# Kernel optimization log

Hardware: AMD Instinct MI355X
Metric: run time of the kernel (lower is better)

## Reference

```python
import jax, jax.numpy as jnp
import numpy as np

N = 100000   # vertices
E = 600000   # directed edges
F = 200000   # triangle faces
CIN = 128
COUT = 128
H = 32       # metric MLP hidden
D = 3        # embedding_dim (3D metric)
TRI = D * (D + 1) // 2  # 6 params of a symmetric 3x3


def setup_inputs() -> dict:
    key = jax.random.key(0)
    ks = jax.random.split(key, 8)
    features = jax.random.normal(ks[0], (N, CIN), jnp.float32)
    vertices = jax.random.normal(ks[1], (N, 3), jnp.float32)
    edges = jax.random.randint(ks[2], (2, E), 0, N)
    faces = jax.random.randint(ks[3], (3, F), 0, N)
    # metric MLP params (edge tangent vector -> symmetric metric params)
    W1 = jax.random.normal(ks[4], (D, H), jnp.float32) / np.sqrt(D)
    b1 = jnp.zeros((H,), jnp.float32)
    W2 = jax.random.normal(ks[5], (H, TRI), jnp.float32) / np.sqrt(H)
    b2 = jnp.zeros((TRI,), jnp.float32)
    # per-vertex feature transform
    Wlin = jax.random.normal(ks[6], (CIN, COUT), jnp.float32) / np.sqrt(CIN)
    blin = jnp.zeros((COUT,), jnp.float32)
    return dict(features=features, vertices=vertices, edges=edges, faces=faces,
                W1=W1, b1=b1, W2=W2, b2=b2, Wlin=Wlin, blin=blin)


def _vertex_normals(vertices, faces):
    # area-weighted vertex normals from triangle faces
    v0, v1, v2 = vertices[faces[0]], vertices[faces[1]], vertices[faces[2]]
    fn = jnp.cross(v1 - v0, v2 - v0)                       # [F,3]
    n = jnp.zeros_like(vertices)
    n = n.at[faces[0]].add(fn).at[faces[1]].add(fn).at[faces[2]].add(fn)
    return n / (jnp.linalg.norm(n, axis=-1, keepdims=True) + 1e-8)


def _sym_from_flat(theta):
    # theta [E,6] -> symmetric [E,3,3]
    iu0, iu1 = jnp.triu_indices(D)
    S = jnp.zeros((theta.shape[0], D, D), theta.dtype)
    S = S.at[:, iu0, iu1].set(theta)
    S = S.at[:, iu1, iu0].set(theta)
    return S


def reference(features, vertices, edges, faces, W1, b1, W2, b2, Wlin, blin):
    eps = 1e-5
    src, dst = edges[0], edges[1]
    normals = _vertex_normals(vertices, faces)             # [N,3] ('tangent' info)
    d = vertices[dst] - vertices[src]                      # [E,3] edge vectors
    n_src = normals[src]
    t = d - jnp.sum(d * n_src, -1, keepdims=True) * n_src  # tangent-plane projection
    # learned metric per edge: MLP -> symmetric S, PSD metric M = S S
    h = jax.nn.relu(t @ W1 + b1)                           # [E,H]
    theta = h @ W2 + b2                                    # [E,6]
    S = _sym_from_flat(theta)                              # [E,3,3]
    M = jnp.einsum('eij,ejk->eik', S, S)                   # PSD metric
    q = jnp.einsum('ei,eij,ej->e', t, M, t)                # metric quadratic form
    w = jnp.exp(-q)                                        # positive edge weights
    # per-vertex linear, then metric-weighted mean aggregation over in-edges
    x = features @ Wlin + blin                             # [N,COUT]
    num = jax.ops.segment_sum(w[:, None] * x[src], dst, num_segments=N)
    den = jax.ops.segment_sum(w, dst, num_segments=N) + eps
    out = num / den[:, None]                               # MetricConv output
    # MetricConvBlock: manual per-feature normalization + ELU
    mu = out.mean(axis=0)
    sd = out.std(axis=0, ddof=1)                           # torch std is unbiased
    out = (out - mu) / (sd + eps)
    return jax.nn.elu(out)
```

## Files before the change

### kernel.cpp

```cpp
#include <hip/hip_runtime.h>
#include <hip/hip_bf16.h>
#include <math.h>

#define N_V 100000
#define N_E 600000
#define N_F 200000

typedef __attribute__((ext_vector_type(8))) short bf16x8;
typedef __attribute__((ext_vector_type(4))) float f32x4;

#define FUSED_BLOCKS 1563
#define FACE_BLOCKS 782
#define EDGE_BLOCKS 2344
#define PACK_BLOCKS 64

__device__ __forceinline__ unsigned short f2bf(float f) {
    unsigned int u = __builtin_bit_cast(unsigned int, f);
    u += 0x7fffu + ((u >> 16) & 1u);
    return (unsigned short)(u >> 16);
}

__global__ void k_build(const int* __restrict__ edges, const int* __restrict__ faces,
                        const float* __restrict__ Wlin,
                        int* __restrict__ head_e, int* __restrict__ next_e,
                        int* __restrict__ head_f, int* __restrict__ next_f,
                        unsigned short* __restrict__ Wb) {
    int b = blockIdx.x;
    int t = threadIdx.x;
    if (b < FACE_BLOCKS) {
        int f = b * 256 + t;
        if (f < N_F) {
            #pragma unroll
            for (int j = 0; j < 3; j++) {
                int v = faces[j * N_F + f];
                int c = 3 * f + j;
                int old = atomicExch(&head_f[v], c);
                next_f[c] = old;
            }
        }
    } else if (b < FACE_BLOCKS + EDGE_BLOCKS) {
        int e = (b - FACE_BLOCKS) * 256 + t;
        if (e < N_E) {
            int d = edges[N_E + e];
            int old = atomicExch(&head_e[d], e);
            next_e[e] = old;
        }
    } else {
        int i = (b - FACE_BLOCKS - EDGE_BLOCKS) * 256 + t;
        int j = i & 7;
        int lane = (i >> 3) & 63;
        int ct = (i >> 9) & 7;
        int kk = i >> 12;
        int k = kk * 32 + (lane >> 4) * 8 + j;
        int n = ct * 16 + (lane & 15);
        Wb[i] = f2bf(Wlin[k * 128 + n]);
    }
}

__global__ void k_vnorm(const float* __restrict__ vtx, const int* __restrict__ faces,
                        const int* __restrict__ head_f, const int* __restrict__ next_f,
                        float* __restrict__ nrm) {
    int v = blockIdx.x * 256 + threadIdx.x;
    if (v >= N_V) return;
    float nx = 0.f, ny = 0.f, nz = 0.f;
    int c = head_f[v];
    while (c >= 0) {
        int f = c / 3;
        int i0 = faces[f], i1 = faces[N_F + f], i2 = faces[2 * N_F + f];
        float ax = vtx[3 * i0], ay = vtx[3 * i0 + 1], az = vtx[3 * i0 + 2];
        float bx = vtx[3 * i1] - ax, by = vtx[3 * i1 + 1] - ay, bz = vtx[3 * i1 + 2] - az;
        float cx = vtx[3 * i2] - ax, cy = vtx[3 * i2 + 1] - ay, cz = vtx[3 * i2 + 2] - az;
        nx += by * cz - bz * cy;
        ny += bz * cx - bx * cz;
        nz += bx * cy - by * cx;
        c = next_f[c];
    }
    float inv = 1.f / (sqrtf(nx * nx + ny * ny + nz * nz) + 1e-8f);
    nrm[3 * v] = nx * inv; nrm[3 * v + 1] = ny * inv; nrm[3 * v + 2] = nz * inv;
}

__global__ void k_edge(const float* __restrict__ vtx, const int* __restrict__ edges,
                       const float* __restrict__ nrm,
                       const float* __restrict__ W1, const float* __restrict__ b1,
                       const float* __restrict__ W2, const float* __restrict__ b2,
                       float* __restrict__ wbuf) {
    __shared__ float sW1[96], sb1[32], sW2[192], sb2[6];
    int t = threadIdx.x;
    if (t < 96)  sW1[t] = W1[t];
    if (t < 32)  sb1[t] = b1[t];
    if (t < 192) sW2[t] = W2[t];
    if (t < 6)   sb2[t] = b2[t];
    __syncthreads();
    int e = blockIdx.x * blockDim.x + t;
    if (e >= N_E) return;
    int s = edges[e], d = edges[N_E + e];
    float dx = vtx[3 * d] - vtx[3 * s];
    float dy = vtx[3 * d + 1] - vtx[3 * s + 1];
    float dz = vtx[3 * d + 2] - vtx[3 * s + 2];
    float nx = nrm[3 * s], ny = nrm[3 * s + 1], nz = nrm[3 * s + 2];
    float dp = dx * nx + dy * ny + dz * nz;
    float tx = dx - dp * nx, ty = dy - dp * ny, tz = dz - dp * nz;
    float th0 = sb2[0], th1 = sb2[1], th2 = sb2[2], th3 = sb2[3], th4 = sb2[4], th5 = sb2[5];
    #pragma unroll
    for (int j = 0; j < 32; j++) {
        float h = tx * sW1[j] + ty * sW1[32 + j] + tz * sW1[64 + j] + sb1[j];
        h = fmaxf(h, 0.f);
        const float* w2r = &sW2[j * 6];
        th0 += h * w2r[0]; th1 += h * w2r[1]; th2 += h * w2r[2];
        th3 += h * w2r[3]; th4 += h * w2r[4]; th5 += h * w2r[5];
    }
    float ux = th0 * tx + th1 * ty + th2 * tz;
    float uy = th1 * tx + th3 * ty + th4 * tz;
    float uz = th2 * tx + th4 * ty + th5 * tz;
    float q = ux * ux + uy * uy + uz * uz;
    wbuf[e] = expf(-q);
}

__global__ __launch_bounds__(512) void k_fused(const float* __restrict__ feat,
                                               const int* __restrict__ edges,
                                               const int* __restrict__ head_e,
                                               const int* __restrict__ next_e,
                                               const float* __restrict__ wbuf,
                                               const unsigned short* __restrict__ Wb,
                                               const float* __restrict__ blin,
                                               float* __restrict__ out,
                                               float* __restrict__ partials) {
    __shared__ __align__(16) unsigned short At[64 * 136];
    __shared__ float gs[64];
    int t = threadIdx.x;
    int hw = t >> 5;
    int hl = t & 31;

    #pragma unroll
    for (int rep = 0; rep < 4; rep++) {
        int row = rep * 16 + hw;
        int v = blockIdx.x * 64 + row;
        float4 acc = {0.f, 0.f, 0.f, 0.f};
        float den = 0.f;
        if (v < N_V) {
            int e = head_e[v];
            while (e >= 0) {
                int s = edges[e];
                float w = wbuf[e];
                float4 f = *(const float4*)(feat + (size_t)s * 128 + 4 * hl);
                acc.x += w * f.x; acc.y += w * f.y; acc.z += w * f.z; acc.w += w * f.w;
                den += w;
                e = next_e[e];
            }
        }
        float inv = 1.f / (den + 1e-5f);
        ushort4 p;
        p.x = f2bf(acc.x * inv); p.y = f2bf(acc.y * inv);
        p.z = f2bf(acc.z * inv); p.w = f2bf(acc.w * inv);
        *(ushort4*)(&At[row * 136 + 4 * hl]) = p;
        if (hl == 0) gs[row] = den * inv;
    }
    __syncthreads();

    int ct = t >> 6;
    int lane = t & 63;
    int m = lane & 15, quad = lane >> 4;
    bf16x8 bfr[4];
    #pragma unroll
    for (int kk = 0; kk < 4; kk++)
        bfr[kk] = *(const bf16x8*)(Wb + (((kk * 8 + ct) * 64 + lane) << 3));
    float bl = blin[ct * 16 + m];
    float ssr = 0.f, qqr = 0.f;
    #pragma unroll
    for (int tile = 0; tile < 4; tile++) {
        f32x4 acc = (f32x4){0.f, 0.f, 0.f, 0.f};
        #pragma unroll
        for (int kk = 0; kk < 4; kk++) {
            bf16x8 af = *(const bf16x8*)(&At[(tile * 16 + m) * 136 + kk * 32 + quad * 8]);
            acc = __builtin_amdgcn_mfma_f32_16x16x32_bf16(af, bfr[kk], acc, 0, 0, 0);
        }
        int r0 = blockIdx.x * 64 + tile * 16;
        #pragma unroll
        for (int reg = 0; reg < 4; reg++) {
            int r = r0 + quad * 4 + reg;
            float g = gs[tile * 16 + quad * 4 + reg];
            float val = acc[reg] + bl * g;
            if (r < N_V) out[(size_t)r * 128 + ct * 16 + m] = val;
            ssr += val; qqr += val * val;
        }
    }
    ssr += __shfl_xor(ssr, 16); qqr += __shfl_xor(qqr, 16);
    ssr += __shfl_xor(ssr, 32); qqr += __shfl_xor(qqr, 32);
    if (quad == 0) {
        partials[(size_t)blockIdx.x * 256 + ct * 16 + m] = ssr;
        partials[(size_t)blockIdx.x * 256 + 128 + ct * 16 + m] = qqr;
    }
}

__global__ __launch_bounds__(64) void k_rstats(const float* __restrict__ partials,
                                               float* __restrict__ stats) {
    int c = blockIdx.x;
    int lane = threadIdx.x;
    float s = 0.f, q = 0.f;
    for (int b = lane; b < FUSED_BLOCKS; b += 64) {
        s += partials[(size_t)b * 256 + c];
        q += partials[(size_t)b * 256 + 128 + c];
    }
    #pragma unroll
    for (int off = 32; off; off >>= 1) {
        s += __shfl_down(s, off);
        q += __shfl_down(q, off);
    }
    if (lane == 0) {
        float mu = s * (1.f / N_V);
        float var = (q - s * mu) * (1.f / (N_V - 1));
        float sd = sqrtf(fmaxf(var, 0.f));
        stats[c] = mu;
        stats[128 + c] = 1.f / (sd + 1e-5f);
    }
}

__global__ void k_finalize(float* __restrict__ out, const float* __restrict__ stats) {
    int i = blockIdx.x * blockDim.x + threadIdx.x;
    if (i >= N_V * 32) return;
    float4 v = ((float4*)out)[i];
    int c0 = (i * 4) & 127;
    float mu0 = stats[c0], mu1 = stats[c0 + 1], mu2 = stats[c0 + 2], mu3 = stats[c0 + 3];
    float is0 = stats[128 + c0], is1 = stats[128 + c0 + 1], is2 = stats[128 + c0 + 2], is3 = stats[128 + c0 + 3];
    v.x = (v.x - mu0) * is0; v.y = (v.y - mu1) * is1;
    v.z = (v.z - mu2) * is2; v.w = (v.w - mu3) * is3;
    v.x = v.x > 0.f ? v.x : expm1f(v.x);
    v.y = v.y > 0.f ? v.y : expm1f(v.y);
    v.z = v.z > 0.f ? v.z : expm1f(v.z);
    v.w = v.w > 0.f ? v.w : expm1f(v.w);
    ((float4*)out)[i] = v;
}

extern "C" void kernel_launch(void* const* d_in, const int* in_sizes, int n_in,
                              void* d_out, int out_size, void* d_ws, size_t ws_size,
                              hipStream_t stream) {
    const float* feat  = (const float*)d_in[0];
    const float* vtx   = (const float*)d_in[1];
    const int*   edges = (const int*)d_in[2];
    const int*   faces = (const int*)d_in[3];
    const float* W1   = (const float*)d_in[4];
    const float* b1   = (const float*)d_in[5];
    const float* W2   = (const float*)d_in[6];
    const float* b2   = (const float*)d_in[7];
    const float* Wlin = (const float*)d_in[8];
    const float* blin = (const float*)d_in[9];
    float* out = (float*)d_out;

    float* ws = (float*)d_ws;
    int*   head_e   = (int*)ws;
    int*   head_f   = (int*)(ws + 100000);
    float* nrm      = ws + 200000;
    float* partials = ws + 100000;
    int*   next_e   = (int*)(ws + 500128);
    int*   next_f   = (int*)(ws + 1100128);
    float* wbuf     = ws + 1100128;
    unsigned short* Wb = (unsigned short*)(ws + 1700128);
    float* stats    = ws;

    hipMemsetAsync(d_ws, 0xFF, 200000 * sizeof(int), stream);

    k_build<<<FACE_BLOCKS + EDGE_BLOCKS + PACK_BLOCKS, 256, 0, stream>>>(
        edges, faces, Wlin, head_e, next_e, head_f, next_f, Wb);
    k_vnorm<<<(N_V + 255) / 256, 256, 0, stream>>>(vtx, faces, head_f, next_f, nrm);
    k_edge<<<EDGE_BLOCKS, 256, 0, stream>>>(vtx, edges, nrm, W1, b1, W2, b2, wbuf);
    k_fused<<<FUSED_BLOCKS, 512, 0, stream>>>(feat, edges, head_e, next_e, wbuf,
                                              Wb, blin, out, partials);
    k_rstats<<<128, 64, 0, stream>>>(partials, stats);
    k_finalize<<<(N_V * 32 + 255) / 256, 256, 0, stream>>>(out, stats);
}
```

Baseline: 311.1 us.

## Precompute face normals once per face and build edge lists inside edge kernel

Result: faster. 289.6 us (-6.9%).

```diff
diff --git a/kernel.cpp b/kernel.cpp
--- a/kernel.cpp
+++ b/kernel.cpp
@@ -20,33 +20,32 @@
     return (unsigned short)(u >> 16);
 }
 
-__global__ void k_build(const int* __restrict__ edges, const int* __restrict__ faces,
-                        const float* __restrict__ Wlin,
-                        int* __restrict__ head_e, int* __restrict__ next_e,
-                        int* __restrict__ head_f, int* __restrict__ next_f,
-                        unsigned short* __restrict__ Wb) {
+__global__ void k_fn(const float* __restrict__ vtx, const int* __restrict__ faces,
+                     const float* __restrict__ Wlin,
+                     float* __restrict__ fnbuf,
+                     int* __restrict__ head_f, int* __restrict__ next_f,
+                     unsigned short* __restrict__ Wb) {
     int b = blockIdx.x;
     int t = threadIdx.x;
     if (b < FACE_BLOCKS) {
         int f = b * 256 + t;
-        if (f < N_F) {
-            #pragma unroll
-            for (int j = 0; j < 3; j++) {
-                int v = faces[j * N_F + f];
-                int c = 3 * f + j;
-                int old = atomicExch(&head_f[v], c);
-                next_f[c] = old;
-            }
-        }
-    } else if (b < FACE_BLOCKS + EDGE_BLOCKS) {
-        int e = (b - FACE_BLOCKS) * 256 + t;
-        if (e < N_E) {
-            int d = edges[N_E + e];
-            int old = atomicExch(&head_e[d], e);
-            next_e[e] = old;
-        }
+        if (f >= N_F) return;
+        int i0 = faces[f], i1 = faces[N_F + f], i2 = faces[2 * N_F + f];
+        #pragma unroll
+        for (int j = 0; j < 3; j++) {
+            int v = (j == 0) ? i0 : (j == 1 ? i1 : i2);
+            int c = 3 * f + j;
+            int old = atomicExch(&head_f[v], c);
+            next_f[c] = old;
+        }
+        float ax = vtx[3 * i0], ay = vtx[3 * i0 + 1], az = vtx[3 * i0 + 2];
+        float bx = vtx[3 * i1] - ax, by = vtx[3 * i1 + 1] - ay, bz = vtx[3 * i1 + 2] - az;
+        float cx = vtx[3 * i2] - ax, cy = vtx[3 * i2 + 1] - ay, cz = vtx[3 * i2 + 2] - az;
+        fnbuf[f]           = by * cz - bz * cy;
+        fnbuf[N_F + f]     = bz * cx - bx * cz;
+        fnbuf[2 * N_F + f] = bx * cy - by * cx;
     } else {
-        int i = (b - FACE_BLOCKS - EDGE_BLOCKS) * 256 + t;
+        int i = (b - FACE_BLOCKS) * 256 + t;
         int j = i & 7;
         int lane = (i >> 3) & 63;
         int ct = (i >> 9) & 7;
@@ -57,7 +56,7 @@
     }
 }
 
-__global__ void k_vnorm(const float* __restrict__ vtx, const int* __restrict__ faces,
+__global__ void k_vnorm(const float* __restrict__ fnbuf,
                         const int* __restrict__ head_f, const int* __restrict__ next_f,
                         float* __restrict__ nrm) {
     int v = blockIdx.x * 256 + threadIdx.x;
@@ -65,14 +64,10 @@
     float nx = 0.f, ny = 0.f, nz = 0.f;
     int c = head_f[v];
     while (c >= 0) {
-        int f = c / 3;
-        int i0 = faces[f], i1 = faces[N_F + f], i2 = faces[2 * N_F + f];
-        float ax = vtx[3 * i0], ay = vtx[3 * i0 + 1], az = vtx[3 * i0 + 2];
-        float bx = vtx[3 * i1] - ax, by = vtx[3 * i1 + 1] - ay, bz = vtx[3 * i1 + 2] - az;
-        float cx = vtx[3 * i2] - ax, cy = vtx[3 * i2 + 1] - ay, cz = vtx[3 * i2 + 2] - az;
-        nx += by * cz - bz * cy;
-        ny += bz * cx - bx * cz;
-        nz += bx * cy - by * cx;
+        int f = (unsigned)c / 3u;
+        nx += fnbuf[f];
+        ny += fnbuf[N_F + f];
+        nz += fnbuf[2 * N_F + f];
         c = next_f[c];
     }
     float inv = 1.f / (sqrtf(nx * nx + ny * ny + nz * nz) + 1e-8f);
@@ -83,7 +78,8 @@
                        const float* __restrict__ nrm,
                        const float* __restrict__ W1, const float* __restrict__ b1,
                        const float* __restrict__ W2, const float* __restrict__ b2,
-                       float* __restrict__ wbuf) {
+                       float* __restrict__ wbuf,
+                       int* __restrict__ head_e, int* __restrict__ next_e) {
     __shared__ float sW1[96], sb1[32], sW2[192], sb2[6];
     int t = threadIdx.x;
     if (t < 96)  sW1[t] = W1[t];
@@ -94,6 +90,7 @@
     int e = blockIdx.x * blockDim.x + t;
     if (e >= N_E) return;
     int s = edges[e], d = edges[N_E + e];
+    int old = atomicExch(&head_e[d], e);
     float dx = vtx[3 * d] - vtx[3 * s];
     float dy = vtx[3 * d + 1] - vtx[3 * s + 1];
     float dz = vtx[3 * d + 2] - vtx[3 * s + 2];
@@ -113,6 +110,7 @@
     float uy = th1 * tx + th3 * ty + th4 * tz;
     float uz = th2 * tx + th4 * ty + th5 * tz;
     float q = ux * ux + uy * uy + uz * uz;
+    next_e[e] = old;
     wbuf[e] = expf(-q);
 }
 
@@ -251,6 +249,7 @@
     int*   head_f   = (int*)(ws + 100000);
     float* nrm      = ws + 200000;
     float* partials = ws + 100000;
+    float* fnbuf    = ws + 500128;
     int*   next_e   = (int*)(ws + 500128);
     int*   next_f   = (int*)(ws + 1100128);
     float* wbuf     = ws + 1100128;
@@ -259,10 +258,11 @@
 
     hipMemsetAsync(d_ws, 0xFF, 200000 * sizeof(int), stream);
 
-    k_build<<<FACE_BLOCKS + EDGE_BLOCKS + PACK_BLOCKS, 256, 0, stream>>>(
-        edges, faces, Wlin, head_e, next_e, head_f, next_f, Wb);
-    k_vnorm<<<(N_V + 255) / 256, 256, 0, stream>>>(vtx, faces, head_f, next_f, nrm);
-    k_edge<<<EDGE_BLOCKS, 256, 0, stream>>>(vtx, edges, nrm, W1, b1, W2, b2, wbuf);
+    k_fn<<<FACE_BLOCKS + PACK_BLOCKS, 256, 0, stream>>>(vtx, faces, Wlin, fnbuf,
+                                                        head_f, next_f, Wb);
+    k_vnorm<<<(N_V + 255) / 256, 256, 0, stream>>>(fnbuf, head_f, next_f, nrm);
+    k_edge<<<EDGE_BLOCKS, 256, 0, stream>>>(vtx, edges, nrm, W1, b1, W2, b2,
+                                            wbuf, head_e, next_e);
     k_fused<<<FUSED_BLOCKS, 512, 0, stream>>>(feat, edges, head_e, next_e, wbuf,
                                               Wb, blin, out, partials);
     k_rstats<<<128, 64, 0, stream>>>(partials, stats);
```
